# Kernel optimization log

Measured on AMD Instinct MI355X. Metric: run time of the kernel, lower is better.

Reference implementation:

```python
import jax, jax.numpy as jnp
import numpy as np

NEG_INF = -1e30
LRELU_SLOPE = 0.01
KEEP_SCALE = 2.0  # 1/(1-p) with p=0.5


def mixed_act(x, tid):
    # x: [B, H], tid: [H] int type ids
    # 0 relu, 1 tanh, 2 sig, 3 'smin'->Softmax, 4 'smax'->Softmin, 5 gelu, 6 lrelu
    relu = jnp.maximum(x, 0.0)
    tanh = jnp.tanh(x)
    sig = jax.nn.sigmoid(x)
    gelu = jax.nn.gelu(x, approximate=False)
    lrelu = jnp.where(x >= 0, x, LRELU_SLOPE * x)
    # softmax/softmin restricted to the columns of that type (matches x[:, idx] gather)
    smin = jax.nn.softmax(jnp.where(tid == 3, x, NEG_INF), axis=1)
    smax = jax.nn.softmax(jnp.where(tid == 4, -x, NEG_INF), axis=1)
    return jnp.select(
        [tid == 0, tid == 1, tid == 2, tid == 3, tid == 4, tid == 5, tid == 6],
        [relu, tanh, sig, smin, smax, gelu, lrelu],
    )


def setup_inputs() -> dict:
    key = jax.random.key(0)
    ks = jax.random.split(key, 16)
    B, D_IN, H, C = 32768, 784, 1024, 10
    s_in, s_h = 1.0 / np.sqrt(D_IN), 1.0 / np.sqrt(H)
    inp = {
        "x": jax.random.normal(ks[0], (B, D_IN), jnp.float32),
        "W0": jax.random.normal(ks[1], (H, D_IN), jnp.float32) * s_in,
        "b0": jax.random.normal(ks[2], (H,), jnp.float32) * s_in,
        "W1": jax.random.normal(ks[3], (H, H), jnp.float32) * s_h,
        "b1": jax.random.normal(ks[4], (H,), jnp.float32) * s_h,
        "W2": jax.random.normal(ks[5], (H, H), jnp.float32) * s_h,
        "b2": jax.random.normal(ks[6], (H,), jnp.float32) * s_h,
        "W3": jax.random.normal(ks[7], (C, H), jnp.float32) * s_h,
        "b3": jax.random.normal(ks[8], (C,), jnp.float32) * s_h,
        "mask1": jax.random.bernoulli(ks[9], 0.5, (B, H)).astype(jnp.float32),
        "mask2": jax.random.bernoulli(ks[10], 0.5, (B, H)).astype(jnp.float32),
        "mask3": jax.random.bernoulli(ks[11], 0.5, (B, H)).astype(jnp.float32),
        "type_ids": jax.random.randint(ks[12], (3, H), 0, 7, jnp.int32),
    }
    return inp


def reference(x, W0, b0, W1, b1, W2, b2, W3, b3, mask1, mask2, mask3, type_ids):
    h = mixed_act(x @ W0.T + b0, type_ids[0])
    h = mixed_act((h * mask1 * KEEP_SCALE) @ W1.T + b1, type_ids[1])
    h = mixed_act((h * mask2 * KEEP_SCALE) @ W2.T + b2, type_ids[2])
    logits = (h * mask3 * KEEP_SCALE) @ W3.T + b3
    out = jax.nn.log_softmax(logits, axis=1)
    return (out, mask1, mask2, mask3)
```

## Files before the change

### kernel.cpp

```cpp
#include <hip/hip_runtime.h>
#include <hip/hip_bf16.h>
#include <cstdint>
#include <cstddef>

typedef __bf16 bf16_t;
typedef bf16_t bf16x8 __attribute__((ext_vector_type(8)));
typedef bf16_t bf16x4 __attribute__((ext_vector_type(4)));
typedef float f32x4 __attribute__((ext_vector_type(4)));

#define NEG_BIG (-1e30f)

__global__ __launch_bounds__(256) void convert_pad(const float* __restrict__ src,
                                                   bf16_t* __restrict__ dst,
                                                   int incols, int outcols) {
    const int row = blockIdx.x;
    const float* s = src + (size_t)row * incols;
    bf16_t* d = dst + (size_t)row * outcols;
    const int n4 = outcols >> 2;
    for (int c = threadIdx.x; c < n4; c += blockDim.x) {
        const int col = c << 2;
        float4 v;
        if (col < incols) v = *(const float4*)(s + col);
        else              v = make_float4(0.f, 0.f, 0.f, 0.f);
        bf16x4 o;
        o[0] = (bf16_t)v.x; o[1] = (bf16_t)v.y; o[2] = (bf16_t)v.z; o[3] = (bf16_t)v.w;
        *(bf16x4*)(d + col) = o;
    }
}

#define BM 128
#define BN 128
#define BK 32

__global__ __launch_bounds__(256) void gemm_bt(const bf16_t* __restrict__ A,
                                               const bf16_t* __restrict__ W,
                                               const float* __restrict__ bias,
                                               bf16_t* __restrict__ Z,
                                               int K, int N) {
    __shared__ __align__(16) bf16_t As[2][BM * BK];
    __shared__ __align__(16) bf16_t Bs[2][BN * BK];
    const int tid  = threadIdx.x;
    const int wid  = tid >> 6;
    const int lane = tid & 63;

    const int bid = (int)blockIdx.x;
    const int cpx = (int)gridDim.x >> 3;
    const int swz = (bid & 7) * cpx + (bid >> 3);
    const int nbn = N >> 7;
    const int n0 = (swz % nbn) * BN;
    const int m0 = (swz / nbn) * BM;

    const int wm = (wid >> 1) * 64;
    const int wn = (wid & 1) * 64;

    f32x4 acc[4][4] = {};

    const int srow = wid * 32 + (lane >> 2);
    const int scol = (((lane & 3) ^ ((lane >> 3) & 3)) << 3);
    const bf16_t* Ap0 = A + (size_t)(m0 + srow) * K + scol;
    const bf16_t* Ap1 = Ap0 + (size_t)16 * K;
    const bf16_t* Wp0 = W + (size_t)(n0 + srow) * K + scol;
    const bf16_t* Wp1 = Wp0 + (size_t)16 * K;

    const int ldsoff = (wid * 2) * 512;

#define STAGE(b, k0)                                                                        \
    do {                                                                                    \
        __builtin_amdgcn_global_load_lds(                                                   \
            (const __attribute__((address_space(1))) void*)(Ap0 + (k0)),                    \
            (__attribute__((address_space(3))) void*)(&As[(b)][ldsoff]), 16, 0, 0);         \
        __builtin_amdgcn_global_load_lds(                                                   \
            (const __attribute__((address_space(1))) void*)(Ap1 + (k0)),                    \
            (__attribute__((address_space(3))) void*)(&As[(b)][ldsoff + 512]), 16, 0, 0);   \
        __builtin_amdgcn_global_load_lds(                                                   \
            (const __attribute__((address_space(1))) void*)(Wp0 + (k0)),                    \
            (__attribute__((address_space(3))) void*)(&Bs[(b)][ldsoff]), 16, 0, 0);         \
        __builtin_amdgcn_global_load_lds(                                                   \
            (const __attribute__((address_space(1))) void*)(Wp1 + (k0)),                    \
            (__attribute__((address_space(3))) void*)(&Bs[(b)][ldsoff + 512]), 16, 0, 0);   \
    } while (0)

    const int nk = K >> 5;
    STAGE(0, 0);
    __syncthreads();

    const int arow = wm + (lane & 15);
    const int brow = wn + (lane & 15);
    const int s    = lane >> 4;
    const int ka   = ((s ^ ((arow >> 1) & 3)) << 3);
    const int kb   = ((s ^ ((brow >> 1) & 3)) << 3);

    int cur = 0;
    for (int t = 0; t < nk; ++t) {
        if (t + 1 < nk) STAGE(cur ^ 1, (t + 1) << 5);

        const bf16_t* Ac = &As[cur][0];
        const bf16_t* Bc = &Bs[cur][0];
        bf16x8 af[4], bfr[4];
        #pragma unroll
        for (int i = 0; i < 4; ++i)
            af[i] = *(const bf16x8*)(Ac + (arow + i * 16) * BK + ka);
        #pragma unroll
        for (int j = 0; j < 4; ++j)
            bfr[j] = *(const bf16x8*)(Bc + (brow + j * 16) * BK + kb);
        #pragma unroll
        for (int i = 0; i < 4; ++i)
            #pragma unroll
            for (int j = 0; j < 4; ++j)
                acc[i][j] = __builtin_amdgcn_mfma_f32_16x16x32_bf16(af[i], bfr[j], acc[i][j], 0, 0, 0);

        __syncthreads();
        cur ^= 1;
    }
#undef STAGE

    const int cq = lane >> 4;
    const int cl = lane & 15;
    #pragma unroll
    for (int j = 0; j < 4; ++j) {
        const int col = n0 + wn + j * 16 + cl;
        const float bj = bias[col];
        #pragma unroll
        for (int i = 0; i < 4; ++i) {
            const int row = m0 + wm + i * 16 + cq * 4;
            #pragma unroll
            for (int r = 0; r < 4; ++r)
                Z[(size_t)(row + r) * N + col] = (bf16_t)(acc[i][j][r] + bj);
        }
    }
}

__global__ __launch_bounds__(256) void act_kernel(const bf16_t* __restrict__ Z,
                                                  const float* __restrict__ mask,
                                                  const int* __restrict__ tids,
                                                  bf16_t* __restrict__ H,
                                                  float* __restrict__ mask_out) {
    const int wid  = threadIdx.x >> 6;
    const int lane = threadIdx.x & 63;
    const int row  = (int)blockIdx.x * 4 + wid;
    const size_t rb = (size_t)row * 1024;

    float p[16], mk[16];
    uint32_t m3 = 0, m4 = 0;
    float s3 = 0.f, s4 = 0.f;

    #pragma unroll
    for (int q = 0; q < 2; ++q) {
        const int c0 = (q * 64 + lane) * 8;
        const bf16x8 z8 = *(const bf16x8*)(Z + rb + c0);
        const int4   ta = *(const int4*)(tids + c0);
        const int4   tb = *(const int4*)(tids + c0 + 4);
        const float4 ma = *(const float4*)(mask + rb + c0);
        const float4 mb = *(const float4*)(mask + rb + c0 + 4);
        const int   tt8[8] = {ta.x, ta.y, ta.z, ta.w, tb.x, tb.y, tb.z, tb.w};
        const float mm8[8] = {ma.x, ma.y, ma.z, ma.w, mb.x, mb.y, mb.z, mb.w};
        #pragma unroll
        for (int j = 0; j < 8; ++j) {
            const int i = q * 8 + j;
            const float zz = (float)z8[j];
            const int tt = tt8[j];
            mk[i] = mm8[j];
            const float az = fabsf(zz);
            const float arg = (tt == 1) ? -2.f * az
                            : (tt == 2) ? -az
                            : (tt == 3) ? zz
                            : (tt == 4) ? -zz : 0.f;
            const float ee = __expf(arg);
            const float r1pe = __builtin_amdgcn_rcpf(1.f + ee);
            const float tha = (1.f - ee) * r1pe;
            const float tnh = (zz >= 0.f) ? tha : -tha;
            const float sg  = ((zz >= 0.f) ? 1.f : ee) * r1pe;
            const float gel = 0.5f * zz * (1.f + erff(zz * 0.70710678f));
            const float pre = (tt == 0) ? fmaxf(zz, 0.f)
                            : (tt == 1) ? tnh
                            : (tt == 2) ? sg
                            : (tt == 3) ? ee
                            : (tt == 4) ? ee
                            : (tt == 5) ? gel
                            : fmaxf(zz, 0.01f * zz);
            p[i] = pre;
            m3 |= (uint32_t)(tt == 3) << i;
            m4 |= (uint32_t)(tt == 4) << i;
            s3 += (tt == 3) ? ee : 0.f;
            s4 += (tt == 4) ? ee : 0.f;
        }
        *(float4*)(mask_out + rb + c0)     = ma;
        *(float4*)(mask_out + rb + c0 + 4) = mb;
    }
    #pragma unroll
    for (int off = 32; off > 0; off >>= 1) {
        s3 += __shfl_xor(s3, off);
        s4 += __shfl_xor(s4, off);
    }
    const float inv3 = 1.f / s3;
    const float inv4 = 1.f / s4;

    #pragma unroll
    for (int q = 0; q < 2; ++q) {
        const int c0 = (q * 64 + lane) * 8;
        bf16x8 h8;
        #pragma unroll
        for (int j = 0; j < 8; ++j) {
            const int i = q * 8 + j;
            const float sc = ((m3 >> i) & 1) ? inv3 : ((m4 >> i) & 1) ? inv4 : 1.f;
            h8[j] = (bf16_t)(p[i] * sc * mk[i] * 2.0f);
        }
        *(bf16x8*)(H + rb + c0) = h8;
    }
}

__global__ __launch_bounds__(256) void act_final(const bf16_t* __restrict__ Z,
                                                 const float* __restrict__ mask,
                                                 const int* __restrict__ tids,
                                                 const bf16_t* __restrict__ W3b,
                                                 const float* __restrict__ b3,
                                                 float* __restrict__ mask_out,
                                                 float* __restrict__ out) {
    __shared__ __align__(16) bf16_t Ws[10 * 1024];
    #pragma unroll
    for (int i = threadIdx.x * 8; i < 10240; i += 2048)
        *(bf16x8*)(Ws + i) = *(const bf16x8*)(W3b + i);
    __syncthreads();

    const int wid  = threadIdx.x >> 6;
    const int lane = threadIdx.x & 63;
    const int row  = (int)blockIdx.x * 4 + wid;
    const size_t rb = (size_t)row * 1024;

    float p[16], mk[16];
    uint32_t m3 = 0, m4 = 0;
    float s3 = 0.f, s4 = 0.f;

    #pragma unroll
    for (int q = 0; q < 2; ++q) {
        const int c0 = (q * 64 + lane) * 8;
        const bf16x8 z8 = *(const bf16x8*)(Z + rb + c0);
        const int4   ta = *(const int4*)(tids + c0);
        const int4   tb = *(const int4*)(tids + c0 + 4);
        const float4 ma = *(const float4*)(mask + rb + c0);
        const float4 mb = *(const float4*)(mask + rb + c0 + 4);
        const int   tt8[8] = {ta.x, ta.y, ta.z, ta.w, tb.x, tb.y, tb.z, tb.w};
        const float mm8[8] = {ma.x, ma.y, ma.z, ma.w, mb.x, mb.y, mb.z, mb.w};
        #pragma unroll
        for (int j = 0; j < 8; ++j) {
            const int i = q * 8 + j;
            const float zz = (float)z8[j];
            const int tt = tt8[j];
            mk[i] = mm8[j];
            const float az = fabsf(zz);
            const float arg = (tt == 1) ? -2.f * az
                            : (tt == 2) ? -az
                            : (tt == 3) ? zz
                            : (tt == 4) ? -zz : 0.f;
            const float ee = __expf(arg);
            const float r1pe = __builtin_amdgcn_rcpf(1.f + ee);
            const float tha = (1.f - ee) * r1pe;
            const float tnh = (zz >= 0.f) ? tha : -tha;
            const float sg  = ((zz >= 0.f) ? 1.f : ee) * r1pe;
            const float gel = 0.5f * zz * (1.f + erff(zz * 0.70710678f));
            const float pre = (tt == 0) ? fmaxf(zz, 0.f)
                            : (tt == 1) ? tnh
                            : (tt == 2) ? sg
                            : (tt == 3) ? ee
                            : (tt == 4) ? ee
                            : (tt == 5) ? gel
                            : fmaxf(zz, 0.01f * zz);
            p[i] = pre;
            m3 |= (uint32_t)(tt == 3) << i;
            m4 |= (uint32_t)(tt == 4) << i;
            s3 += (tt == 3) ? ee : 0.f;
            s4 += (tt == 4) ? ee : 0.f;
        }
        *(float4*)(mask_out + rb + c0)     = ma;
        *(float4*)(mask_out + rb + c0 + 4) = mb;
    }
    #pragma unroll
    for (int off = 32; off > 0; off >>= 1) {
        s3 += __shfl_xor(s3, off);
        s4 += __shfl_xor(s4, off);
    }
    const float inv3 = 1.f / s3;
    const float inv4 = 1.f / s4;

    float acc[10];
    #pragma unroll
    for (int n = 0; n < 10; ++n) acc[n] = 0.f;

    #pragma unroll
    for (int q = 0; q < 2; ++q) {
        const int c0 = (q * 64 + lane) * 8;
        float h[8];
        #pragma unroll
        for (int j = 0; j < 8; ++j) {
            const int i = q * 8 + j;
            const float sc = ((m3 >> i) & 1) ? inv3 : ((m4 >> i) & 1) ? inv4 : 1.f;
            h[j] = p[i] * sc * mk[i] * 2.0f;
        }
        #pragma unroll
        for (int n = 0; n < 10; ++n) {
            const bf16x8 w8 = *(const bf16x8*)(Ws + n * 1024 + c0);
            float d = 0.f;
            #pragma unroll
            for (int j = 0; j < 8; ++j) d += h[j] * (float)w8[j];
            acc[n] += d;
        }
    }

    #pragma unroll
    for (int n = 0; n < 10; ++n)
        #pragma unroll
        for (int off = 32; off > 0; off >>= 1)
            acc[n] += __shfl_xor(acc[n], off);

    if (lane == 0) {
        float lg[10]; float mx = -1e30f;
        #pragma unroll
        for (int n = 0; n < 10; ++n) { lg[n] = acc[n] + b3[n]; mx = fmaxf(mx, lg[n]); }
        float se = 0.f;
        #pragma unroll
        for (int n = 0; n < 10; ++n) se += __expf(lg[n] - mx);
        const float lse = logf(se) + mx;
        #pragma unroll
        for (int n = 0; n < 10; ++n) out[(size_t)row * 10 + n] = lg[n] - lse;
    }
}

extern "C" void kernel_launch(void* const* d_in, const int* in_sizes, int n_in,
                              void* d_out, int out_size, void* d_ws, size_t ws_size,
                              hipStream_t stream) {
    (void)in_sizes; (void)n_in; (void)out_size; (void)ws_size;
    const float* x     = (const float*)d_in[0];
    const float* W0    = (const float*)d_in[1];
    const float* b0    = (const float*)d_in[2];
    const float* W1    = (const float*)d_in[3];
    const float* b1    = (const float*)d_in[4];
    const float* W2    = (const float*)d_in[5];
    const float* b2    = (const float*)d_in[6];
    const float* W3    = (const float*)d_in[7];
    const float* b3    = (const float*)d_in[8];
    const float* mask1 = (const float*)d_in[9];
    const float* mask2 = (const float*)d_in[10];
    const float* mask3 = (const float*)d_in[11];
    const int*   tids  = (const int*)d_in[12];

    float* out = (float*)d_out;
    float* mo1 = out + 327680;
    float* mo2 = mo1 + 33554432;
    float* mo3 = mo2 + 33554432;

    char* ws = (char*)d_ws;
    bf16_t* xb  = (bf16_t*)ws;  ws += (size_t)32768 * 800 * 2;
    bf16_t* W0b = (bf16_t*)ws;  ws += (size_t)1024 * 800 * 2;
    bf16_t* W1b = (bf16_t*)ws;  ws += (size_t)1024 * 1024 * 2;
    bf16_t* W2b = (bf16_t*)ws;  ws += (size_t)1024 * 1024 * 2;
    bf16_t* W3b = (bf16_t*)ws;  ws += (size_t)16 * 1024 * 2;
    bf16_t* Zb  = (bf16_t*)ws;  ws += (size_t)32768 * 1024 * 2;
    bf16_t* hb  = (bf16_t*)ws;  ws += (size_t)32768 * 1024 * 2;

    convert_pad<<<32768, 256, 0, stream>>>(x,  xb,  784, 800);
    convert_pad<<<1024,  256, 0, stream>>>(W0, W0b, 784, 800);
    convert_pad<<<1024,  256, 0, stream>>>(W1, W1b, 1024, 1024);
    convert_pad<<<1024,  256, 0, stream>>>(W2, W2b, 1024, 1024);
    convert_pad<<<10,    256, 0, stream>>>(W3, W3b, 1024, 1024);

    gemm_bt<<<2048, 256, 0, stream>>>(xb, W0b, b0, Zb, 800, 1024);
    act_kernel<<<8192, 256, 0, stream>>>(Zb, mask1, tids, hb, mo1);
    gemm_bt<<<2048, 256, 0, stream>>>(hb, W1b, b1, Zb, 1024, 1024);
    act_kernel<<<8192, 256, 0, stream>>>(Zb, mask2, tids + 1024, hb, mo2);
    gemm_bt<<<2048, 256, 0, stream>>>(hb, W2b, b2, Zb, 1024, 1024);
    act_final<<<8192, 256, 0, stream>>>(Zb, mask3, tids + 2048, W3b, b3, mo3, out);
}
```

Before: 1.118 ms.

## Enlarge GEMM tile to 128x256 with triple-buffered LDS and staged epilogue

Widens the GEMM block tile to 128x256, so each wave computes 128x64 with 32 accumulators, and halves the grid. The LDS pipeline goes from double to triple buffering, using explicit vmcnt waits and raw barriers in place of __syncthreads. The epilogue stages outputs through swizzled LDS so each thread writes full 16-byte rows instead of scattered 2-byte stores. The aim is more MFMA work per byte loaded, better latency hiding and coalesced stores, at the cost of more registers and LDS (73 KB), which can lower occupancy.

```diff
diff --git a/kernel.cpp b/kernel.cpp
--- a/kernel.cpp
+++ b/kernel.cpp
@@ -29,16 +29,16 @@
 }
 
 #define BM 128
-#define BN 128
+#define BN 256
 #define BK 32
 
-__global__ __launch_bounds__(256) void gemm_bt(const bf16_t* __restrict__ A,
-                                               const bf16_t* __restrict__ W,
-                                               const float* __restrict__ bias,
-                                               bf16_t* __restrict__ Z,
-                                               int K, int N) {
-    __shared__ __align__(16) bf16_t As[2][BM * BK];
-    __shared__ __align__(16) bf16_t Bs[2][BN * BK];
+__global__ __launch_bounds__(256, 2) void gemm_bt(const bf16_t* __restrict__ A,
+                                                  const bf16_t* __restrict__ W,
+                                                  const float* __restrict__ bias,
+                                                  bf16_t* __restrict__ Z,
+                                                  int K, int N) {
+    __shared__ __align__(16) char smem[73728];
+    bf16_t* sb = (bf16_t*)smem;
     const int tid  = threadIdx.x;
     const int wid  = tid >> 6;
     const int lane = tid & 63;
@@ -46,71 +46,86 @@
     const int bid = (int)blockIdx.x;
     const int cpx = (int)gridDim.x >> 3;
     const int swz = (bid & 7) * cpx + (bid >> 3);
-    const int nbn = N >> 7;
+    const int nbn = N >> 8;
     const int n0 = (swz % nbn) * BN;
     const int m0 = (swz / nbn) * BM;
 
-    const int wm = (wid >> 1) * 64;
-    const int wn = (wid & 1) * 64;
-
-    f32x4 acc[4][4] = {};
-
-    const int srow = wid * 32 + (lane >> 2);
+    f32x4 acc[8][4] = {};
+
+    const int srA  = lane >> 2;
     const int scol = (((lane & 3) ^ ((lane >> 3) & 3)) << 3);
-    const bf16_t* Ap0 = A + (size_t)(m0 + srow) * K + scol;
-    const bf16_t* Ap1 = Ap0 + (size_t)16 * K;
-    const bf16_t* Wp0 = W + (size_t)(n0 + srow) * K + scol;
-    const bf16_t* Wp1 = Wp0 + (size_t)16 * K;
-
-    const int ldsoff = (wid * 2) * 512;
-
-#define STAGE(b, k0)                                                                        \
-    do {                                                                                    \
-        __builtin_amdgcn_global_load_lds(                                                   \
-            (const __attribute__((address_space(1))) void*)(Ap0 + (k0)),                    \
-            (__attribute__((address_space(3))) void*)(&As[(b)][ldsoff]), 16, 0, 0);         \
-        __builtin_amdgcn_global_load_lds(                                                   \
-            (const __attribute__((address_space(1))) void*)(Ap1 + (k0)),                    \
-            (__attribute__((address_space(3))) void*)(&As[(b)][ldsoff + 512]), 16, 0, 0);   \
-        __builtin_amdgcn_global_load_lds(                                                   \
-            (const __attribute__((address_space(1))) void*)(Wp0 + (k0)),                    \
-            (__attribute__((address_space(3))) void*)(&Bs[(b)][ldsoff]), 16, 0, 0);         \
-        __builtin_amdgcn_global_load_lds(                                                   \
-            (const __attribute__((address_space(1))) void*)(Wp1 + (k0)),                    \
-            (__attribute__((address_space(3))) void*)(&Bs[(b)][ldsoff + 512]), 16, 0, 0);   \
+    const bf16_t* Ap = A + (size_t)(m0 + wid * 32 + srA) * K + scol;
+    const bf16_t* Wp = W + (size_t)(n0 + wid * 64 + srA) * K + scol;
+    const size_t K16 = (size_t)16 * K;
+
+    const int aoff = (wid * 2) * 512;
+    const int boff = 4096 + (wid * 4) * 512;
+
+#define STAGE(b, kt)                                                                          \
+    do {                                                                                      \
+        const int k0_ = (kt) * BK;                                                            \
+        bf16_t* dst_ = sb + (b) * 12288;                                                      \
+        __builtin_amdgcn_global_load_lds(                                                     \
+            (const __attribute__((address_space(1))) void*)(Ap + k0_),                        \
+            (__attribute__((address_space(3))) void*)(dst_ + aoff), 16, 0, 0);                \
+        __builtin_amdgcn_global_load_lds(                                                     \
+            (const __attribute__((address_space(1))) void*)(Ap + k0_ + K16),                  \
+            (__attribute__((address_space(3))) void*)(dst_ + aoff + 512), 16, 0, 0);          \
+        __builtin_amdgcn_global_load_lds(                                                     \
+            (const __attribute__((address_space(1))) void*)(Wp + k0_),                        \
+            (__attribute__((address_space(3))) void*)(dst_ + boff), 16, 0, 0);                \
+        __builtin_amdgcn_global_load_lds(                                                     \
+            (const __attribute__((address_space(1))) void*)(Wp + k0_ + K16),                  \
+            (__attribute__((address_space(3))) void*)(dst_ + boff + 512), 16, 0, 0);          \
+        __builtin_amdgcn_global_load_lds(                                                     \
+            (const __attribute__((address_space(1))) void*)(Wp + k0_ + 2 * K16),              \
+            (__attribute__((address_space(3))) void*)(dst_ + boff + 1024), 16, 0, 0);         \
+        __builtin_amdgcn_global_load_lds(                                                     \
+            (const __attribute__((address_space(1))) void*)(Wp + k0_ + 3 * K16),              \
+            (__attribute__((address_space(3))) void*)(dst_ + boff + 1536), 16, 0, 0);         \
     } while (0)
 
     const int nk = K >> 5;
     STAGE(0, 0);
-    __syncthreads();
-
-    const int arow = wm + (lane & 15);
-    const int brow = wn + (lane & 15);
-    const int s    = lane >> 4;
-    const int ka   = ((s ^ ((arow >> 1) & 3)) << 3);
-    const int kb   = ((s ^ ((brow >> 1) & 3)) << 3);
-
-    int cur = 0;
+    STAGE(1, 1);
+    asm volatile("s_waitcnt vmcnt(6)" ::: "memory");
+    __builtin_amdgcn_s_barrier();
+    asm volatile("" ::: "memory");
+
+    const int ar = lane & 15;
+    const int br = wid * 64 + (lane & 15);
+    const int s_ = lane >> 4;
+    const int ka = ((s_ ^ ((ar >> 1) & 3)) << 3);
+    const int kb = ((s_ ^ ((br >> 1) & 3)) << 3);
+
+    int cb = 0;
+    int pb = 2;
     for (int t = 0; t < nk; ++t) {
-        if (t + 1 < nk) STAGE(cur ^ 1, (t + 1) << 5);
-
-        const bf16_t* Ac = &As[cur][0];
-        const bf16_t* Bc = &Bs[cur][0];
-        bf16x8 af[4], bfr[4];
-        #pragma unroll
-        for (int i = 0; i < 4; ++i)
-            af[i] = *(const bf16x8*)(Ac + (arow + i * 16) * BK + ka);
+        if (t + 2 < nk) STAGE(pb, t + 2);
+
+        const bf16_t* As_ = sb + cb * 12288;
+        const bf16_t* Bs_ = As_ + 4096;
+        bf16x8 af[8], bfr[4];
         #pragma unroll
         for (int j = 0; j < 4; ++j)
-            bfr[j] = *(const bf16x8*)(Bc + (brow + j * 16) * BK + kb);
-        #pragma unroll
-        for (int i = 0; i < 4; ++i)
+            bfr[j] = *(const bf16x8*)(Bs_ + (br + j * 16) * 32 + kb);
+        #pragma unroll
+        for (int i = 0; i < 8; ++i)
+            af[i] = *(const bf16x8*)(As_ + (ar + i * 16) * 32 + ka);
+        #pragma unroll
+        for (int i = 0; i < 8; ++i)
             #pragma unroll
             for (int j = 0; j < 4; ++j)
                 acc[i][j] = __builtin_amdgcn_mfma_f32_16x16x32_bf16(af[i], bfr[j], acc[i][j], 0, 0, 0);
 
-        __syncthreads();
-        cur ^= 1;
+        asm volatile("s_waitcnt lgkmcnt(0)" ::: "memory");
+        if (t + 2 < nk) asm volatile("s_waitcnt vmcnt(6)" ::: "memory");
+        else            asm volatile("s_waitcnt vmcnt(0)" ::: "memory");
+        __builtin_amdgcn_s_barrier();
+        asm volatile("" ::: "memory");
+
+        cb = (cb == 2) ? 0 : cb + 1;
+        pb = (pb == 2) ? 0 : pb + 1;
     }
 #undef STAGE
 
@@ -118,15 +133,26 @@
     const int cl = lane & 15;
     #pragma unroll
     for (int j = 0; j < 4; ++j) {
-        const int col = n0 + wn + j * 16 + cl;
-        const float bj = bias[col];
-        #pragma unroll
-        for (int i = 0; i < 4; ++i) {
-            const int row = m0 + wm + i * 16 + cq * 4;
+        const int col = wid * 64 + j * 16 + cl;
+        const float bj = bias[n0 + col];
+        #pragma unroll
+        for (int i = 0; i < 8; ++i) {
             #pragma unroll
-            for (int r = 0; r < 4; ++r)
-                Z[(size_t)(row + r) * N + col] = (bf16_t)(acc[i][j][r] + bj);
-        }
+            for (int r = 0; r < 4; ++r) {
+                const int row = i * 16 + cq * 4 + r;
+                const int bo = (row * 512 + col * 2) ^ ((row & 7) << 4);
+                *(bf16_t*)(smem + bo) = (bf16_t)(acc[i][j][r] + bj);
+            }
+        }
+    }
+    __syncthreads();
+    #pragma unroll
+    for (int p = 0; p < 16; ++p) {
+        const int row  = p * 8 + (tid >> 5);
+        const int slot = tid & 31;
+        const int bo = (row * 512 + slot * 16) ^ ((row & 7) << 4);
+        const bf16x8 v = *(const bf16x8*)(smem + bo);
+        *(bf16x8*)(Z + (size_t)(m0 + row) * N + n0 + slot * 8) = v;
     }
 }
 
@@ -363,10 +389,10 @@
     convert_pad<<<1024,  256, 0, stream>>>(W2, W2b, 1024, 1024);
     convert_pad<<<10,    256, 0, stream>>>(W3, W3b, 1024, 1024);
 
-    gemm_bt<<<2048, 256, 0, stream>>>(xb, W0b, b0, Zb, 800, 1024);
+    gemm_bt<<<1024, 256, 0, stream>>>(xb, W0b, b0, Zb, 800, 1024);
     act_kernel<<<8192, 256, 0, stream>>>(Zb, mask1, tids, hb, mo1);
-    gemm_bt<<<2048, 256, 0, stream>>>(hb, W1b, b1, Zb, 1024, 1024);
+    gemm_bt<<<1024, 256, 0, stream>>>(hb, W1b, b1, Zb, 1024, 1024);
     act_kernel<<<8192, 256, 0, stream>>>(Zb, mask2, tids + 1024, hb, mo2);
-    gemm_bt<<<2048, 256, 0, stream>>>(hb, W2b, b2, Zb, 1024, 1024);
+    gemm_bt<<<1024, 256, 0, stream>>>(hb, W2b, b2, Zb, 1024, 1024);
     act_final<<<8192, 256, 0, stream>>>(Zb, mask3, tids + 2048, W3b, b3, mo3, out);
 }
```

Result: faster. 1.068 ms (-4.5%).
